# Performance work log

Hardware: AMD Instinct MI355X
Metric: run time of the kernel (lower is better)

Reference implementation:

```python
import jax, jax.numpy as jnp
import numpy as np

B, L, D, H, V = 128, 512, 300, 200, 50000
NEG_INF = 1e12  # constant.INFINITY_NUMBER in the source repo


def setup_inputs() -> dict:
    key = jax.random.key(0)
    ks = jax.random.split(key, 12)
    words = jax.random.randint(ks[0], (B, L), 0, V)
    subj_pos = jax.random.randint(ks[1], (B, L), 0, 8)
    obj_pos = jax.random.randint(ks[2], (B, L), 0, 8)
    emb_table = jax.random.uniform(ks[3], (V, D), jnp.float32, -1.0, 1.0)
    emb_table = emb_table.at[0].set(0.0)  # padding_idx = 0
    s = 0.05
    w1 = jax.random.normal(ks[4], (2 * D, H), jnp.float32) * s   # attn fc layer 1
    b1 = jnp.zeros((H,), jnp.float32)
    w2 = jax.random.normal(ks[5], (H, 1), jnp.float32) * s       # attn fc layer 2
    b2 = jnp.zeros((1,), jnp.float32)
    mw1 = jax.random.normal(ks[6], (4 * D, H), jnp.float32) * s  # out_mlp layer 1 (in_dim=1200)
    mb1 = jnp.zeros((H,), jnp.float32)
    mw2 = jax.random.normal(ks[7], (H, H), jnp.float32) * s      # out_mlp layer 2
    mb2 = jnp.zeros((H,), jnp.float32)
    return {"words": words, "subj_pos": subj_pos, "obj_pos": obj_pos,
            "emb_table": emb_table, "w1": w1, "b1": b1, "w2": w2, "b2": b2,
            "mw1": mw1, "mb1": mb1, "mw2": mw2, "mb2": mb2}


def _masked_max_pool(h, mask):
    # mask: [B,L,1] True where position should be suppressed
    return jnp.max(jnp.where(mask, -NEG_INF, h), axis=1)


def _attention_net(prefs, supervisor, w1, b1, w2, b2):
    # vectorized version of the per-position loop:
    # score[b,i] = W2 @ tanh(W1 @ cat(prefs[b,i], supervisor[b]) + b1) + b2
    sup = jnp.broadcast_to(supervisor[:, None, :], prefs.shape)  # [B,L,D]
    cat = jnp.concatenate([prefs, sup], axis=-1)                 # [B,L,2D]
    hid = jnp.tanh(jnp.einsum('blk,kh->blh', cat, w1) + b1)
    scores = (jnp.einsum('blh,ho->blo', hid, w2) + b2)[..., 0]   # [B,L]
    attn = jax.nn.softmax(scores, axis=1)
    return jnp.einsum('bld,bl->bd', prefs, attn)                 # [B,D]


def reference(words, subj_pos, obj_pos, emb_table, w1, b1, w2, b2, mw1, mb1, mw2, mb2):
    word_emb = emb_table[words]                                  # [B,L,D]
    subj_mask = (subj_pos != 0)[:, :, None]
    obj_mask = (obj_pos != 0)[:, :, None]
    subj_emb = _masked_max_pool(word_emb, subj_mask)             # [B,D]
    obj_emb = _masked_max_pool(word_emb, obj_mask)               # [B,D]
    # NOTE: source bug — obj_attn also uses subj_emb and subj_attn_fc.
    subj_attn = _attention_net(word_emb, subj_emb, w1, b1, w2, b2)
    obj_attn = _attention_net(word_emb, subj_emb, w1, b1, w2, b2)
    out = jnp.concatenate([subj_attn, obj_attn, subj_emb, obj_emb], axis=1)  # [B,4D]
    out = jax.nn.relu(out @ mw1 + mb1)
    out = jax.nn.relu(out @ mw2 + mb2)
    return out
```

## Files before the change

kernel.cpp:

```cpp
#include <hip/hip_runtime.h>
#include <hip/hip_bf16.h>

#define BB 128
#define LL 512
#define DD 300
#define HH 200
#define VV 50000
#define KP 320
#define NEGBIG 1e12f

typedef __attribute__((ext_vector_type(8))) short bf16x8;
typedef __attribute__((ext_vector_type(4))) float f32x4;

__device__ __forceinline__ float bf2f(unsigned short u) {
  union { unsigned int i; float f; } v; v.i = ((unsigned int)u) << 16; return v.f;
}
__device__ __forceinline__ unsigned short f2bf(float f) {
  union { float f; unsigned int i; } v; v.f = f;
  unsigned int r = v.i + 0x7FFFu + ((v.i >> 16) & 1u);
  return (unsigned short)(r >> 16);
}

typedef const __attribute__((address_space(1))) unsigned int ga_u32;
typedef __attribute__((address_space(3))) unsigned int lds_u32;
__device__ __forceinline__ void gl_lds16(const void* g, void* l) {
  __builtin_amdgcn_global_load_lds((ga_u32*)g, (lds_u32*)l, 16, 0, 0);
}

__global__ __launch_bounds__(256) void gather_pool(
    const int* __restrict__ words, const int* __restrict__ spos,
    const int* __restrict__ opos, const float* __restrict__ tab,
    const float* __restrict__ w1,
    unsigned short* __restrict__ embbf, unsigned short* __restrict__ w1s2,
    float* __restrict__ spart, float* __restrict__ opart) {
  int blk = blockIdx.x;
  int tid = threadIdx.x;

  if (blk >= 1024) {
    int u = (blk - 1024) * 256 + tid;
    int kc = u >> 10;
    int rem = u & 1023;
    int row = rem >> 2, c16 = rem & 3;
    int s = (row ^ (row >> 2)) & 3;
    int kb = kc * 32 + ((c16 ^ s) << 3);
    bf16x8 o;
#pragma unroll
    for (int j = 0; j < 8; ++j) {
      int k = kb + j;
      float v = (k < DD && row < HH) ? w1[(size_t)k * HH + row] : 0.f;
      o[j] = (short)f2bf(v);
    }
    *(bf16x8*)(w1s2 + (size_t)u * 8) = o;
    return;
  }

  int b = blk >> 3, ch = blk & 7, l0 = ch * 64;
  __shared__ int wd[64], sm[64], om[64];
  __shared__ unsigned short tile[64 * 328];
  if (tid < 64) {
    wd[tid] = words[b * LL + l0 + tid];
    sm[tid] = spos[b * LL + l0 + tid];
    om[tid] = opos[b * LL + l0 + tid];
  }
  __syncthreads();

  {
    int r = tid >> 2, qg = tid & 3;
    const float* srow = tab + (size_t)wd[r] * DD;
    unsigned short* trow = tile + r * 328;
#pragma unroll
    for (int i = 0; i < 19; ++i) {
      int q = qg + 4 * i;
      if (q < 75) {
        float4 v = *(const float4*)(srow + q * 4);
        ushort4 o;
        o.x = f2bf(v.x); o.y = f2bf(v.y); o.z = f2bf(v.z); o.w = f2bf(v.w);
        *(ushort4*)(trow + q * 4) = o;
      }
    }
    if (qg == 0) {
#pragma unroll
      for (int c = 300; c < 328; c += 4) {
        ushort4 z; z.x = z.y = z.z = z.w = 0;
        *(ushort4*)(trow + c) = z;
      }
    }
  }
  __syncthreads();

  {
    char* embdst = (char*)embbf + (size_t)(b * LL + l0) * 640;
#pragma unroll
    for (int j = 0; j < 10; ++j) {
      int g16 = j * 256 + tid;
      int row = g16 / 40, cb = g16 % 40;
      uint4 v = *(const uint4*)((const char*)tile + row * 656 + cb * 16);
      *(uint4*)(embdst + (size_t)g16 * 16) = v;
    }
  }

  if (tid < 150) {
    float s0 = -NEGBIG, s1 = -NEGBIG, o0 = -NEGBIG, o1 = -NEGBIG;
    for (int r = 0; r < 64; ++r) {
      unsigned int v = *(const unsigned int*)((const char*)tile + r * 656 + tid * 4);
      float v0 = bf2f((unsigned short)(v & 0xffff));
      float v1 = bf2f((unsigned short)(v >> 16));
      if (sm[r] == 0) { s0 = fmaxf(s0, v0); s1 = fmaxf(s1, v1); }
      if (om[r] == 0) { o0 = fmaxf(o0, v0); o1 = fmaxf(o1, v1); }
    }
    size_t base = (size_t)(ch * BB + b) * DD + tid * 2;
    *(float2*)(spart + base) = make_float2(s0, s1);
    *(float2*)(opart + base) = make_float2(o0, o1);
  }
}

__global__ __launch_bounds__(320) void combine_preh(
    const float* __restrict__ spart, const float* __restrict__ opart,
    const float* __restrict__ w1, const float* __restrict__ b1,
    float* __restrict__ semb, float* __restrict__ oemb,
    float* __restrict__ preh) {
  int b = blockIdx.x, t = threadIdx.x;
  __shared__ float se[DD];
  if (t < DD) {
    float s = -NEGBIG, o = -NEGBIG;
    for (int ch = 0; ch < 8; ++ch) {
      size_t base = (size_t)(ch * BB + b) * DD + t;
      s = fmaxf(s, spart[base]);
      o = fmaxf(o, opart[base]);
    }
    semb[(size_t)b * DD + t] = s;
    oemb[(size_t)b * DD + t] = o;
    se[t] = s;
  }
  __syncthreads();
  if (t < HH) {
    float acc = b1[t];
    for (int d = 0; d < DD; ++d) acc += se[d] * w1[(size_t)(DD + d) * HH + t];
    preh[(size_t)b * HH + t] = acc;
  }
}

__global__ __launch_bounds__(256) void scores_mfma(
    const unsigned short* __restrict__ embbf,
    const unsigned short* __restrict__ w1s2, const float* __restrict__ preh,
    const float* __restrict__ w2, const float* __restrict__ b2,
    float* __restrict__ scores) {
  int tile = blockIdx.x;
  int b = tile >> 3, l0 = (tile & 7) * 64;
  int tid = threadIdx.x;
  int w = tid >> 6, lane = tid & 63;
  int lr = lane & 15, lq = lane >> 4;

  __shared__ unsigned short ldsA[64 * 320];
  __shared__ unsigned short ldsB[2][256 * 32];

  const char* embbase = (const char*)embbf + (size_t)(b * LL + l0) * 640;
  int wbase16 = (w << 6);

#pragma unroll
  for (int j = 0; j < 10; ++j) {
    int d16 = j * 256 + tid;
    int row = d16 / 40, c = d16 % 40;
    const void* src = embbase + row * 640 + (c ^ (row & 7)) * 16;
    void* dst = (char*)ldsA + (size_t)(j * 256 + wbase16) * 16;
    gl_lds16(src, dst);
  }
  {
    const char* srcb = (const char*)w1s2;
#pragma unroll
    for (int j = 0; j < 4; ++j)
      gl_lds16(srcb + (size_t)(j * 256 + tid) * 16,
               (char*)&ldsB[0][0] + (size_t)(j * 256 + wbase16) * 16);
  }
  __syncthreads();

  f32x4 acc[13];
#pragma unroll
  for (int nt = 0; nt < 13; ++nt) acc[nt] = (f32x4){0.f, 0.f, 0.f, 0.f};

  int slr = (lr ^ (lr >> 2)) & 3;
  const char* aAddr = (const char*)ldsA + (w * 16 + lr) * 640;
  int cur = 0;
  for (int kc = 0; kc < 10; ++kc) {
    if (kc < 9) {
      const char* srcb = (const char*)w1s2 + (size_t)(kc + 1) * 16384;
#pragma unroll
      for (int j = 0; j < 4; ++j)
        gl_lds16(srcb + (size_t)(j * 256 + tid) * 16,
                 (char*)&ldsB[cur ^ 1][0] + (size_t)(j * 256 + wbase16) * 16);
    }
    bf16x8 a = *(const bf16x8*)(aAddr + (((kc * 4 + lq) ^ (lr & 7)) * 16));
    const char* bbase = (const char*)&ldsB[cur][0] + lr * 64 + ((lq ^ slr) * 16);
#pragma unroll
    for (int nt = 0; nt < 13; ++nt) {
      bf16x8 bv = *(const bf16x8*)(bbase + nt * 16 * 64);
      acc[nt] = __builtin_amdgcn_mfma_f32_16x16x32_bf16(a, bv, acc[nt], 0, 0, 0);
    }
    __syncthreads();
    cur ^= 1;
  }

  float w2v[13], ph[13];
#pragma unroll
  for (int nt = 0; nt < 13; ++nt) {
    int h = nt * 16 + lr;
    bool v = (h < HH);
    w2v[nt] = v ? w2[h] : 0.f;
    ph[nt] = v ? preh[(size_t)b * HH + h] : 0.f;
  }
  float part[4] = {0.f, 0.f, 0.f, 0.f};
#pragma unroll
  for (int nt = 0; nt < 13; ++nt) {
#pragma unroll
    for (int r = 0; r < 4; ++r)
      part[r] += w2v[nt] * tanhf(acc[nt][r] + ph[nt]);
  }
#pragma unroll
  for (int off = 8; off; off >>= 1) {
#pragma unroll
    for (int r = 0; r < 4; ++r) part[r] += __shfl_xor(part[r], off, 16);
  }
  if (lr == 0) {
    float bb = b2[0];
#pragma unroll
    for (int r = 0; r < 4; ++r) {
      int pos = l0 + w * 16 + lq * 4 + r;
      scores[(size_t)b * LL + pos] = part[r] + bb;
    }
  }
}

__global__ __launch_bounds__(256) void pv_sm(
    const float* __restrict__ scores, const unsigned short* __restrict__ embbf,
    float* __restrict__ avpart) {
  int blk = blockIdx.x;
  int b = blk >> 3, ch = blk & 7, l0 = ch * 64;
  int tid = threadIdx.x;
  __shared__ float red[16];
  __shared__ float at[64];

  float s0 = scores[(size_t)b * LL + tid];
  float s1 = scores[(size_t)b * LL + 256 + tid];
  float m = fmaxf(s0, s1);
#pragma unroll
  for (int off = 32; off; off >>= 1) m = fmaxf(m, __shfl_xor(m, off, 64));
  if ((tid & 63) == 0) red[tid >> 6] = m;
  __syncthreads();
  float M = fmaxf(fmaxf(red[0], red[1]), fmaxf(red[2], red[3]));
  float e = expf(s0 - M) + expf(s1 - M);
#pragma unroll
  for (int off = 32; off; off >>= 1) e += __shfl_xor(e, off, 64);
  if ((tid & 63) == 0) red[8 + (tid >> 6)] = e;
  __syncthreads();
  float S = red[8] + red[9] + red[10] + red[11];
  if (tid < 64) at[tid] = expf(scores[(size_t)b * LL + l0 + tid] - M) / S;
  __syncthreads();

  if (tid >= 150) return;
  const char* base = (const char*)embbf + (size_t)(b * LL + l0) * 640 + tid * 4;
  float a0 = 0.f, a1 = 0.f;
  for (int r = 0; r < 64; ++r) {
    unsigned int v = *(const unsigned int*)(base + (size_t)r * 640);
    float wgt = at[r];
    a0 += wgt * bf2f((unsigned short)(v & 0xffff));
    a1 += wgt * bf2f((unsigned short)(v >> 16));
  }
  size_t obase = (size_t)(ch * BB + b) * DD + tid * 2;
  *(float2*)(avpart + obase) = make_float2(a0, a1);
}

__global__ __launch_bounds__(256) void mlp_fused(
    const float* __restrict__ avpart, const float* __restrict__ semb,
    const float* __restrict__ oemb, const float* __restrict__ mw1,
    const float* __restrict__ mb1, const float* __restrict__ mw2,
    const float* __restrict__ mb2, float* __restrict__ out) {
  int b0 = blockIdx.x * 4;
  int tid = threadIdx.x;
  __shared__ float x[4][1200];
  __shared__ float h1[4][HH];

  for (int idx = tid; idx < 4800; idx += 256) {
    int bb = idx / 1200, k = idx - bb * 1200;
    int b = b0 + bb;
    float v;
    if (k < 600) {
      int d = (k >= DD) ? k - DD : k;
      v = 0.f;
#pragma unroll
      for (int chh = 0; chh < 8; ++chh)
        v += avpart[(size_t)(chh * BB + b) * DD + d];
    } else if (k < 900) {
      v = semb[(size_t)b * DD + (k - 600)];
    } else {
      v = oemb[(size_t)b * DD + (k - 900)];
    }
    x[bb][k] = v;
  }
  __syncthreads();

  if (tid < HH) {
    float acc[4];
#pragma unroll
    for (int bb = 0; bb < 4; ++bb) acc[bb] = mb1[tid];
    for (int k = 0; k < 1200; ++k) {
      float wv = mw1[(size_t)k * HH + tid];
#pragma unroll
      for (int bb = 0; bb < 4; ++bb) acc[bb] += x[bb][k] * wv;
    }
#pragma unroll
    for (int bb = 0; bb < 4; ++bb) h1[bb][tid] = fmaxf(acc[bb], 0.f);
  }
  __syncthreads();
  if (tid < HH) {
    float acc[4];
#pragma unroll
    for (int bb = 0; bb < 4; ++bb) acc[bb] = mb2[tid];
    for (int k = 0; k < HH; ++k) {
      float wv = mw2[(size_t)k * HH + tid];
#pragma unroll
      for (int bb = 0; bb < 4; ++bb) acc[bb] += h1[bb][k] * wv;
    }
#pragma unroll
    for (int bb = 0; bb < 4; ++bb)
      out[(size_t)(b0 + bb) * HH + tid] = fmaxf(acc[bb], 0.f);
  }
}

extern "C" void kernel_launch(void* const* d_in, const int* in_sizes, int n_in,
                              void* d_out, int out_size, void* d_ws, size_t ws_size,
                              hipStream_t stream) {
  const int* words = (const int*)d_in[0];
  const int* spos  = (const int*)d_in[1];
  const int* opos  = (const int*)d_in[2];
  const float* tab = (const float*)d_in[3];
  const float* w1  = (const float*)d_in[4];
  const float* b1  = (const float*)d_in[5];
  const float* w2  = (const float*)d_in[6];
  const float* b2  = (const float*)d_in[7];
  const float* mw1 = (const float*)d_in[8];
  const float* mb1 = (const float*)d_in[9];
  const float* mw2 = (const float*)d_in[10];
  const float* mb2 = (const float*)d_in[11];
  float* out = (float*)d_out;

  char* p = (char*)d_ws;
  unsigned short* embbf = (unsigned short*)p; p += (size_t)BB * LL * KP * 2;
  unsigned short* w1s2  = (unsigned short*)p; p += (size_t)10 * 256 * 4 * 16;
  float* spart  = (float*)p; p += (size_t)8 * BB * DD * 4;
  float* opart  = (float*)p; p += (size_t)8 * BB * DD * 4;
  float* avpart = (float*)p; p += (size_t)8 * BB * DD * 4;
  float* semb   = (float*)p; p += (size_t)BB * DD * 4;
  float* oemb   = (float*)p; p += (size_t)BB * DD * 4;
  float* preh   = (float*)p; p += (size_t)BB * HH * 4;
  float* scores = (float*)p; p += (size_t)BB * LL * 4;

  gather_pool<<<dim3(1064), dim3(256), 0, stream>>>(
      words, spos, opos, tab, w1, embbf, w1s2, spart, opart);
  combine_preh<<<dim3(BB), dim3(320), 0, stream>>>(
      spart, opart, w1, b1, semb, oemb, preh);
  scores_mfma<<<dim3(BB * 8), dim3(256), 0, stream>>>(
      embbf, w1s2, preh, w2, b2, scores);
  pv_sm<<<dim3(BB * 8), dim3(256), 0, stream>>>(scores, embbf, avpart);
  mlp_fused<<<dim3(32), dim3(256), 0, stream>>>(
      avpart, semb, oemb, mw1, mb1, mw2, mb2, out);
}
```

Before: 235.9 us.

## Fold duplicate attention weights and split output MLP into split-K partial kernels

Since subj_attn and obj_attn are identical, the two matching row blocks of the first MLP weight are summed into an effective 900-row matrix inside the gather kernel's extra blocks, which removes a quarter of the first layer's multiply work. The output MLP, which ran on only 32 blocks, becomes a split-K kernel of 288 blocks writing partial sums, followed by a per-batch kernel that reduces them, applies ReLU and runs the second layer. The preh loop is also unrolled. In exchange the pipeline gains an extra launch and a partial-sum buffer in global memory, and the gather grid grows by about 700 blocks to precompute the folded weights.

```diff
diff --git a/kernel.cpp b/kernel.cpp
--- a/kernel.cpp
+++ b/kernel.cpp
@@ -30,12 +30,25 @@
 __global__ __launch_bounds__(256) void gather_pool(
     const int* __restrict__ words, const int* __restrict__ spos,
     const int* __restrict__ opos, const float* __restrict__ tab,
-    const float* __restrict__ w1,
+    const float* __restrict__ w1, const float* __restrict__ mw1,
     unsigned short* __restrict__ embbf, unsigned short* __restrict__ w1s2,
+    float* __restrict__ mw1eff,
     float* __restrict__ spart, float* __restrict__ opart) {
   int blk = blockIdx.x;
   int tid = threadIdx.x;
 
+  if (blk >= 1064) {
+    int idx = (blk - 1064) * 256 + tid;
+    if (idx < 900 * HH) {
+      int k = idx / HH, h = idx - k * HH;
+      float v;
+      if (k < 300) v = mw1[(size_t)k * HH + h] + mw1[(size_t)(300 + k) * HH + h];
+      else if (k < 600) v = mw1[(size_t)(k + 300) * HH + h];
+      else v = mw1[(size_t)(k + 300) * HH + h];
+      mw1eff[idx] = v;
+    }
+    return;
+  }
   if (blk >= 1024) {
     int u = (blk - 1024) * 256 + tid;
     int kc = u >> 10;
@@ -134,8 +147,10 @@
   }
   __syncthreads();
   if (t < HH) {
+    const float* w1b = w1 + (size_t)DD * HH + t;
     float acc = b1[t];
-    for (int d = 0; d < DD; ++d) acc += se[d] * w1[(size_t)(DD + d) * HH + t];
+#pragma unroll 10
+    for (int d = 0; d < DD; ++d) acc += se[d] * w1b[(size_t)d * HH];
     preh[(size_t)b * HH + t] = acc;
   }
 }
@@ -269,61 +284,66 @@
   *(float2*)(avpart + obase) = make_float2(a0, a1);
 }
 
-__global__ __launch_bounds__(256) void mlp_fused(
+__global__ __launch_bounds__(256) void mlp1p(
     const float* __restrict__ avpart, const float* __restrict__ semb,
-    const float* __restrict__ oemb, const float* __restrict__ mw1,
-    const float* __restrict__ mb1, const float* __restrict__ mw2,
-    const float* __restrict__ mb2, float* __restrict__ out) {
-  int b0 = blockIdx.x * 4;
+    const float* __restrict__ oemb, const float* __restrict__ mw1eff,
+    float* __restrict__ p1) {
+  int bc = blockIdx.x / 18, kc = blockIdx.x % 18;
   int tid = threadIdx.x;
-  __shared__ float x[4][1200];
-  __shared__ float h1[4][HH];
-
-  for (int idx = tid; idx < 4800; idx += 256) {
-    int bb = idx / 1200, k = idx - bb * 1200;
-    int b = b0 + bb;
+  __shared__ float xT[50][8];
+  for (int idx = tid; idx < 400; idx += 256) {
+    int bb = idx & 7, kk = idx >> 3;
+    int k = kc * 50 + kk;
+    int b = bc * 8 + bb;
+    int reg = k / 300, d = k - reg * 300;
     float v;
-    if (k < 600) {
-      int d = (k >= DD) ? k - DD : k;
+    if (reg == 0) {
       v = 0.f;
 #pragma unroll
       for (int chh = 0; chh < 8; ++chh)
         v += avpart[(size_t)(chh * BB + b) * DD + d];
-    } else if (k < 900) {
-      v = semb[(size_t)b * DD + (k - 600)];
+    } else if (reg == 1) {
+      v = semb[(size_t)b * DD + d];
     } else {
-      v = oemb[(size_t)b * DD + (k - 900)];
-    }
-    x[bb][k] = v;
-  }
-  __syncthreads();
-
+      v = oemb[(size_t)b * DD + d];
+    }
+    xT[kk][bb] = v;
+  }
+  __syncthreads();
+  if (tid >= HH) return;
+  const float* wp = mw1eff + (size_t)(kc * 50) * HH + tid;
+  float acc[8] = {0.f, 0.f, 0.f, 0.f, 0.f, 0.f, 0.f, 0.f};
+#pragma unroll 5
+  for (int kk = 0; kk < 50; ++kk) {
+    float wv = wp[(size_t)kk * HH];
+#pragma unroll
+    for (int bb = 0; bb < 8; ++bb) acc[bb] += xT[kk][bb] * wv;
+  }
+#pragma unroll
+  for (int bb = 0; bb < 8; ++bb)
+    p1[((size_t)kc * BB + bc * 8 + bb) * HH + tid] = acc[bb];
+}
+
+__global__ __launch_bounds__(256) void mlp2f(
+    const float* __restrict__ p1, const float* __restrict__ mb1,
+    const float* __restrict__ mw2, const float* __restrict__ mb2,
+    float* __restrict__ out) {
+  int b = blockIdx.x, tid = threadIdx.x;
+  __shared__ float h1[HH];
   if (tid < HH) {
-    float acc[4];
-#pragma unroll
-    for (int bb = 0; bb < 4; ++bb) acc[bb] = mb1[tid];
-    for (int k = 0; k < 1200; ++k) {
-      float wv = mw1[(size_t)k * HH + tid];
-#pragma unroll
-      for (int bb = 0; bb < 4; ++bb) acc[bb] += x[bb][k] * wv;
-    }
-#pragma unroll
-    for (int bb = 0; bb < 4; ++bb) h1[bb][tid] = fmaxf(acc[bb], 0.f);
-  }
-  __syncthreads();
-  if (tid < HH) {
-    float acc[4];
-#pragma unroll
-    for (int bb = 0; bb < 4; ++bb) acc[bb] = mb2[tid];
-    for (int k = 0; k < HH; ++k) {
-      float wv = mw2[(size_t)k * HH + tid];
-#pragma unroll
-      for (int bb = 0; bb < 4; ++bb) acc[bb] += h1[bb][k] * wv;
-    }
-#pragma unroll
-    for (int bb = 0; bb < 4; ++bb)
-      out[(size_t)(b0 + bb) * HH + tid] = fmaxf(acc[bb], 0.f);
-  }
+    float s = mb1[tid];
+#pragma unroll
+    for (int kc = 0; kc < 18; ++kc)
+      s += p1[((size_t)kc * BB + b) * HH + tid];
+    h1[tid] = fmaxf(s, 0.f);
+  }
+  __syncthreads();
+  if (tid >= HH) return;
+  const float* wp = mw2 + tid;
+  float acc = mb2[tid];
+#pragma unroll 8
+  for (int k = 0; k < HH; ++k) acc += h1[k] * wp[(size_t)k * HH];
+  out[(size_t)b * HH + tid] = fmaxf(acc, 0.f);
 }
 
 extern "C" void kernel_launch(void* const* d_in, const int* in_sizes, int n_in,
@@ -346,6 +366,7 @@
   char* p = (char*)d_ws;
   unsigned short* embbf = (unsigned short*)p; p += (size_t)BB * LL * KP * 2;
   unsigned short* w1s2  = (unsigned short*)p; p += (size_t)10 * 256 * 4 * 16;
+  float* mw1eff = (float*)p; p += (size_t)900 * HH * 4;
   float* spart  = (float*)p; p += (size_t)8 * BB * DD * 4;
   float* opart  = (float*)p; p += (size_t)8 * BB * DD * 4;
   float* avpart = (float*)p; p += (size_t)8 * BB * DD * 4;
@@ -353,14 +374,15 @@
   float* oemb   = (float*)p; p += (size_t)BB * DD * 4;
   float* preh   = (float*)p; p += (size_t)BB * HH * 4;
   float* scores = (float*)p; p += (size_t)BB * LL * 4;
-
-  gather_pool<<<dim3(1064), dim3(256), 0, stream>>>(
-      words, spos, opos, tab, w1, embbf, w1s2, spart, opart);
+  float* p1     = (float*)p; p += (size_t)18 * BB * HH * 4;
+
+  gather_pool<<<dim3(1768), dim3(256), 0, stream>>>(
+      words, spos, opos, tab, w1, mw1, embbf, w1s2, mw1eff, spart, opart);
   combine_preh<<<dim3(BB), dim3(320), 0, stream>>>(
       spart, opart, w1, b1, semb, oemb, preh);
   scores_mfma<<<dim3(BB * 8), dim3(256), 0, stream>>>(
       embbf, w1s2, preh, w2, b2, scores);
   pv_sm<<<dim3(BB * 8), dim3(256), 0, stream>>>(scores, embbf, avpart);
-  mlp_fused<<<dim3(32), dim3(256), 0, stream>>>(
-      avpart, semb, oemb, mw1, mb1, mw2, mb2, out);
-}
+  mlp1p<<<dim3(288), dim3(256), 0, stream>>>(avpart, semb, oemb, mw1eff, p1);
+  mlp2f<<<dim3(BB), dim3(256), 0, stream>>>(p1, mb1, mw2, mb2, out);
+}
```

Result: faster. 206.8 us (-12.3%).
